# Optimization experiments

Hardware: AMD Instinct MI355X
Metric: run time of the kernel (lower is better)

The kernel has to match this reference:

```python
import jax, jax.numpy as jnp
import numpy as np

N, E, D = 100000, 1600000, 128


def setup_inputs() -> dict:
    key = jax.random.key(0)
    ks = jax.random.split(key, 8)
    s = 1.0 / np.sqrt(D)
    return {
        "x": jax.random.normal(ks[0], (N, D), dtype=jnp.float32),
        "edge_index": jax.random.randint(ks[1], (2, E), 0, N, dtype=jnp.int64),
        "x_prev": jax.random.normal(ks[2], (N, D), dtype=jnp.float32),
        # GCNConv params: weight [in,out], bias [out]
        "W": jax.random.uniform(ks[3], (D, D), jnp.float32, -s, s),
        "b": jnp.zeros((D,), jnp.float32),
        # GRUCell params (torch layout): [3*H, H] gates ordered (r, z, n)
        "W_ih": jax.random.uniform(ks[4], (3 * D, D), jnp.float32, -s, s),
        "W_hh": jax.random.uniform(ks[5], (3 * D, D), jnp.float32, -s, s),
        "b_ih": jax.random.uniform(ks[6], (3 * D,), jnp.float32, -s, s),
        "b_hh": jax.random.uniform(ks[7], (3 * D,), jnp.float32, -s, s),
    }


def _gcn_conv(x, edge_index, W, b):
    n = x.shape[0]
    loop = jnp.arange(n, dtype=edge_index.dtype)
    src = jnp.concatenate([edge_index[0], loop])  # [E+N]
    dst = jnp.concatenate([edge_index[1], loop])
    # symmetric normalization: deg over destinations (incl. self loops)
    deg = jax.ops.segment_sum(jnp.ones_like(dst, dtype=x.dtype), dst, num_segments=n)
    dinv = jnp.where(deg > 0, jax.lax.rsqrt(deg), 0.0)
    norm = dinv[src] * dinv[dst]  # [E+N]
    xw = x @ W  # [N, out]
    msg = xw[src] * norm[:, None]  # gather + scale
    return jax.ops.segment_sum(msg, dst, num_segments=n) + b


def _gru_cell(inp, h, W_ih, W_hh, b_ih, b_hh):
    gi = inp @ W_ih.T + b_ih  # [N, 3H]
    gh = h @ W_hh.T + b_hh
    i_r, i_z, i_n = jnp.split(gi, 3, axis=-1)
    h_r, h_z, h_n = jnp.split(gh, 3, axis=-1)
    r = jax.nn.sigmoid(i_r + h_r)
    z = jax.nn.sigmoid(i_z + h_z)
    ntil = jnp.tanh(i_n + r * h_n)
    return (1.0 - z) * ntil + z * h


def reference(x, edge_index, x_prev, W, b, W_ih, W_hh, b_ih, b_hh):
    h_cur = _gcn_conv(x, edge_index, W, b)
    return _gru_cell(h_cur, x_prev, W_ih, W_hh, b_ih, b_hh)
```

## Files before the change

kernel.cpp:

```cpp
#include <hip/hip_runtime.h>
#include <hip/hip_bf16.h>
#include <math.h>

#define DIM 128
#define PSHIFT 10
#define PSZ 1024
#define CHUNK 2048

typedef __attribute__((ext_vector_type(8))) short bf16x8;
typedef __attribute__((ext_vector_type(4))) float f32x4;
typedef unsigned short u16;
typedef unsigned int u32;
typedef unsigned long long u64;

__device__ __forceinline__ u16 f2bf(float x) {
    u32 u = __builtin_bit_cast(u32, x);
    u += 0x7fff + ((u >> 16) & 1);
    return (u16)(u >> 16);
}
__device__ __forceinline__ float bf2f(u16 h) {
    return __builtin_bit_cast(float, (u32)h << 16);
}


__global__ __launch_bounds__(256) void k_zero(int* __restrict__ p, int n) {
    int i = blockIdx.x * 256 + threadIdx.x;
    if (i < n) p[i] = 0;
}

__global__ __launch_bounds__(256) void k_pcount(const int* __restrict__ edst,
                                                int* __restrict__ pcnt, int E) {
    __shared__ int h[128];
    int t = threadIdx.x;
    if (t < 128) h[t] = 0;
    __syncthreads();
    int stride = gridDim.x * 256;
    for (int e = blockIdx.x * 256 + t; e < E; e += stride)
        atomicAdd(&h[edst[e] >> PSHIFT], 1);
    __syncthreads();
    if (t < 128 && h[t]) atomicAdd(&pcnt[t], h[t]);
}

__global__ __launch_bounds__(256) void k_pscan(const int* __restrict__ pcnt,
                                               int* __restrict__ poff,
                                               int* __restrict__ pfill,
                                               int* __restrict__ rowp,
                                               int P, int N, int E) {
    __shared__ int a[256];
    int t = threadIdx.x;
    int v = (t < P) ? pcnt[t] : 0;
    a[t] = v;
    __syncthreads();
    #pragma unroll
    for (int off = 1; off < 256; off <<= 1) {
        int y = (t >= off) ? a[t - off] : 0;
        __syncthreads();
        a[t] += y;
        __syncthreads();
    }
    int excl = a[t] - v;
    if (t < P) { poff[t] = excl; pfill[t] = excl; }
    if (t == 0) { poff[P] = E; rowp[N] = E; }
}

__global__ __launch_bounds__(256) void k_pscatter(const int* __restrict__ esrc,
                                                  const int* __restrict__ edst,
                                                  int* __restrict__ pfill,
                                                  u64* __restrict__ pbuf, int E) {
    __shared__ int hist[128], sc[128], lofs[128], gbase[128];
    __shared__ u32 ss[CHUNK], sd[CHUNK];
    int t = threadIdx.x;
    int c0 = blockIdx.x * CHUNK;
    int cnt = E - c0; if (cnt > CHUNK) cnt = CHUNK;

    if (t < 128) hist[t] = 0;
    __syncthreads();

    u32 s[8], d[8];
    int p[8], r[8];
    #pragma unroll
    for (int j = 0; j < 8; ++j) {
        int i = j * 256 + t;
        if (i < cnt) {
            s[j] = (u32)esrc[c0 + i];
            d[j] = (u32)edst[c0 + i];
            p[j] = (int)(d[j] >> PSHIFT);
            r[j] = atomicAdd(&hist[p[j]], 1);
        }
    }
    __syncthreads();

    if (t < 128) sc[t] = hist[t];
    __syncthreads();
    #pragma unroll
    for (int off = 1; off < 128; off <<= 1) {
        int y = 0;
        if (t < 128 && t >= off) y = sc[t - off];
        __syncthreads();
        if (t < 128) sc[t] += y;
        __syncthreads();
    }
    if (t < 128) {
        lofs[t] = sc[t] - hist[t];
        if (hist[t] > 0) gbase[t] = atomicAdd(&pfill[t], hist[t]);
    }
    __syncthreads();

    #pragma unroll
    for (int j = 0; j < 8; ++j) {
        int i = j * 256 + t;
        if (i < cnt) {
            int idx = lofs[p[j]] + r[j];
            ss[idx] = s[j];
            sd[idx] = d[j];
        }
    }
    __syncthreads();

    for (int i = t; i < cnt; i += 256) {
        u32 dd = sd[i];
        int pp = (int)(dd >> PSHIFT);
        int gpos = gbase[pp] + (i - lofs[pp]);
        pbuf[gpos] = (u64)ss[i] | ((u64)dd << 32);
    }
}

__global__ __launch_bounds__(256) void k_pfill(const u64* __restrict__ pbuf,
                                               const int* __restrict__ poff,
                                               int* __restrict__ rowp,
                                               int* __restrict__ srcs,
                                               float* __restrict__ dinv, int N) {
    __shared__ int cnt[PSZ];
    __shared__ int wsum[4];
    int p = blockIdx.x, t = threadIdx.x;
    int lane = t & 63, wid = t >> 6;
    int nb0 = p << PSHIFT;
    int ncnt = N - nb0; if (ncnt > PSZ) ncnt = PSZ;
    int b0 = poff[p], b1 = poff[p + 1];
    int bc = b1 - b0;

    for (int i = t; i < PSZ; i += 256) cnt[i] = 0;
    __syncthreads();
    for (int i = t; i < bc; i += 256) {
        u32 d = (u32)(pbuf[b0 + i] >> 32);
        atomicAdd(&cnt[d - nb0], 1);
    }
    __syncthreads();

    int base = t * 4;
    int c[4];
    int ssum = 0;
    #pragma unroll
    for (int j = 0; j < 4; ++j) { c[j] = cnt[base + j]; ssum += c[j]; }
    int incl = ssum;
    #pragma unroll
    for (int off = 1; off < 64; off <<= 1) {
        int y = __shfl_up(incl, off, 64);
        if (lane >= off) incl += y;
    }
    if (lane == 63) wsum[wid] = incl;
    __syncthreads();
    int add = 0;
    for (int w = 0; w < wid; ++w) add += wsum[w];
    int rr = b0 + add + (incl - ssum);
    #pragma unroll
    for (int j = 0; j < 4; ++j) {
        int i = base + j;
        if (i < ncnt) {
            rowp[nb0 + i] = rr;
            dinv[nb0 + i] = rsqrtf((float)(c[j] + 1));
        }
        cnt[i] = rr;
        rr += c[j];
    }
    __syncthreads();

    for (int i = t; i < bc; i += 256) {
        u64 v = pbuf[b0 + i];
        u32 sv = (u32)v;
        u32 d = (u32)(v >> 32);
        int pos = atomicAdd(&cnt[d - nb0], 1);
        srcs[pos] = (int)sv;
    }
}


__global__ __launch_bounds__(256) void k_prepw(const float* __restrict__ W,
                                               const float* __restrict__ Wih,
                                               const float* __restrict__ Whh,
                                               u16* __restrict__ Wt,
                                               u16* __restrict__ Wihb,
                                               u16* __restrict__ Whhb) {
    int i = blockIdx.x * 256 + threadIdx.x;
    if (i < 128 * 128) {
        int k = i >> 7, c = i & 127;
        Wt[c * 128 + k] = f2bf(W[i]);
    }
    if (i < 3 * 128 * 128) {
        Wihb[i] = f2bf(Wih[i]);
        Whhb[i] = f2bf(Whh[i]);
    }
}

__global__ __launch_bounds__(256) void k_cast1(const float4* __restrict__ a,
                                               u32* __restrict__ ab, int n4) {
    int stride = gridDim.x * 256;
    for (int i = blockIdx.x * 256 + threadIdx.x; i < n4; i += stride) {
        float4 v = a[i];
        ab[i * 2 + 0] = (u32)f2bf(v.x) | ((u32)f2bf(v.y) << 16);
        ab[i * 2 + 1] = (u32)f2bf(v.z) | ((u32)f2bf(v.w) << 16);
    }
}


__global__ __launch_bounds__(256) void k_gemm1(const float* __restrict__ X,
                                               const u16* __restrict__ Wt,
                                               u16* __restrict__ XWb, int n) {
    __shared__ u16 Wlds[128 * 128];
    int t = threadIdx.x, w = t >> 6, l = t & 63;
    int lr = l & 15, q = l >> 4;

    for (int cidx = t; cidx < 2048; cidx += 256) {
        int r = cidx >> 4, kc = cidx & 15;
        int dst = r * 128 + ((kc * 8) ^ ((r & 7) << 3));
        *(bf16x8*)(Wlds + dst) = *(const bf16x8*)(Wt + r * 128 + kc * 8);
    }
    __syncthreads();

    int r0 = blockIdx.x * 128;
    int wrow0 = r0 + w * 32;
    int sw = (lr & 7) << 3;
    int ar0 = wrow0 + lr;      if (ar0 > n - 1) ar0 = n - 1;
    int ar1 = wrow0 + 16 + lr; if (ar1 > n - 1) ar1 = n - 1;
    const float* x0 = X + (size_t)ar0 * DIM;
    const float* x1 = X + (size_t)ar1 * DIM;

    f32x4 acc[2][8];
    #pragma unroll
    for (int s = 0; s < 2; ++s)
        #pragma unroll
        for (int c = 0; c < 8; ++c) acc[s][c] = (f32x4){0.f, 0.f, 0.f, 0.f};

    #pragma unroll
    for (int kb = 0; kb < 4; ++kb) {
        int ko = kb * 32 + q * 8;
        float4 f00 = *(const float4*)(x0 + ko), f01 = *(const float4*)(x0 + ko + 4);
        float4 f10 = *(const float4*)(x1 + ko), f11 = *(const float4*)(x1 + ko + 4);
        bf16x8 a0, a1;
        a0[0] = (short)f2bf(f00.x); a0[1] = (short)f2bf(f00.y);
        a0[2] = (short)f2bf(f00.z); a0[3] = (short)f2bf(f00.w);
        a0[4] = (short)f2bf(f01.x); a0[5] = (short)f2bf(f01.y);
        a0[6] = (short)f2bf(f01.z); a0[7] = (short)f2bf(f01.w);
        a1[0] = (short)f2bf(f10.x); a1[1] = (short)f2bf(f10.y);
        a1[2] = (short)f2bf(f10.z); a1[3] = (short)f2bf(f10.w);
        a1[4] = (short)f2bf(f11.x); a1[5] = (short)f2bf(f11.y);
        a1[6] = (short)f2bf(f11.z); a1[7] = (short)f2bf(f11.w);
        int kw = ko ^ sw;
        #pragma unroll
        for (int ct = 0; ct < 8; ++ct) {
            bf16x8 b = *(const bf16x8*)(Wlds + (ct * 16 + lr) * 128 + kw);
            acc[0][ct] = __builtin_amdgcn_mfma_f32_16x16x32_bf16(a0, b, acc[0][ct], 0, 0, 0);
            acc[1][ct] = __builtin_amdgcn_mfma_f32_16x16x32_bf16(a1, b, acc[1][ct], 0, 0, 0);
        }
    }

    #pragma unroll
    for (int s = 0; s < 2; ++s)
        #pragma unroll
        for (int ct = 0; ct < 8; ++ct)
            #pragma unroll
            for (int i = 0; i < 4; ++i) {
                int row = wrow0 + s * 16 + q * 4 + i;
                if (row < n)
                    XWb[(size_t)row * DIM + ct * 16 + lr] = f2bf(acc[s][ct][i]);
            }
}


__global__ __launch_bounds__(256) void k_gather(const u16* __restrict__ XWb,
                                                const float* __restrict__ dinv,
                                                const int* __restrict__ row_ptr,
                                                const int* __restrict__ srcs,
                                                const float* __restrict__ bias,
                                                u16* __restrict__ Hcb, int n) {
    int node = blockIdx.x * 4 + (threadIdx.x >> 6);
    if (node >= n) return;
    int lane = threadIdx.x & 63;
    int c = lane * 2;

    float di = dinv[node];
    u32 sv = *(const u32*)(XWb + (size_t)node * DIM + c);
    float accx = bias[c]     + bf2f((u16)(sv & 0xffff)) * di * di;
    float accy = bias[c + 1] + bf2f((u16)(sv >> 16))    * di * di;

    int e = row_ptr[node], end = row_ptr[node + 1];
    for (; e + 3 < end; e += 4) {
        int s0 = srcs[e], s1 = srcs[e + 1], s2 = srcs[e + 2], s3 = srcs[e + 3];
        float n0 = dinv[s0] * di, n1 = dinv[s1] * di, n2 = dinv[s2] * di, n3 = dinv[s3] * di;
        u32 v0 = *(const u32*)(XWb + (size_t)s0 * DIM + c);
        u32 v1 = *(const u32*)(XWb + (size_t)s1 * DIM + c);
        u32 v2 = *(const u32*)(XWb + (size_t)s2 * DIM + c);
        u32 v3 = *(const u32*)(XWb + (size_t)s3 * DIM + c);
        accx += bf2f((u16)(v0 & 0xffff)) * n0 + bf2f((u16)(v1 & 0xffff)) * n1
              + bf2f((u16)(v2 & 0xffff)) * n2 + bf2f((u16)(v3 & 0xffff)) * n3;
        accy += bf2f((u16)(v0 >> 16)) * n0 + bf2f((u16)(v1 >> 16)) * n1
              + bf2f((u16)(v2 >> 16)) * n2 + bf2f((u16)(v3 >> 16)) * n3;
    }
    for (; e < end; ++e) {
        int s = srcs[e];
        float nrm = dinv[s] * di;
        u32 v = *(const u32*)(XWb + (size_t)s * DIM + c);
        accx += bf2f((u16)(v & 0xffff)) * nrm;
        accy += bf2f((u16)(v >> 16)) * nrm;
    }
    *(u32*)(Hcb + (size_t)node * DIM + c) = (u32)f2bf(accx) | ((u32)f2bf(accy) << 16);
}


__global__ __launch_bounds__(256) void k_gru(const u16* __restrict__ Hcb,
                                             const u16* __restrict__ Xpb,
                                             const u16* __restrict__ Wihb,
                                             const u16* __restrict__ Whhb,
                                             const float* __restrict__ bih,
                                             const float* __restrict__ bhh,
                                             float* __restrict__ Out, int n) {
    __shared__ u16 Wlds[192 * 128];
    int t = threadIdx.x, w = t >> 6, l = t & 63;
    int lr = l & 15, q = l >> 4;
    int cs = blockIdx.x & 3;
    int rb = blockIdx.x >> 2;
    int c0 = cs * 32;
    int r0 = rb * 128;

    for (int cidx = t; cidx < 3072; cidx += 256) {
        int r = cidx >> 4, kc = cidx & 15;
        int m = (r >= 96);
        int rr = m ? r - 96 : r;
        int g = rr >> 5, cc = rr & 31;
        const u16* src = (m ? Whhb : Wihb) + (size_t)((g << 7) + c0 + cc) * DIM + kc * 8;
        int dst = r * 128 + ((kc * 8) ^ ((r & 7) << 3));
        *(bf16x8*)(Wlds + dst) = *(const bf16x8*)src;
    }
    __syncthreads();

    int wrow0 = r0 + w * 32;
    int sw = (lr & 7) << 3;
    int ar0 = wrow0 + lr;      if (ar0 > n - 1) ar0 = n - 1;
    int ar1 = wrow0 + 16 + lr; if (ar1 > n - 1) ar1 = n - 1;
    const u16* hb0 = Hcb + (size_t)ar0 * DIM;
    const u16* hb1 = Hcb + (size_t)ar1 * DIM;
    const u16* xb0 = Xpb + (size_t)ar0 * DIM;
    const u16* xb1 = Xpb + (size_t)ar1 * DIM;

    f32x4 aI[3][2][2], aH[3][2][2];
    #pragma unroll
    for (int g = 0; g < 3; ++g)
        #pragma unroll
        for (int s = 0; s < 2; ++s)
            #pragma unroll
            for (int c = 0; c < 2; ++c) {
                aI[g][s][c] = (f32x4){0.f, 0.f, 0.f, 0.f};
                aH[g][s][c] = (f32x4){0.f, 0.f, 0.f, 0.f};
            }

    #pragma unroll
    for (int kb = 0; kb < 4; ++kb) {
        int ko = kb * 32 + q * 8;
        bf16x8 hA0 = *(const bf16x8*)(hb0 + ko);
        bf16x8 hA1 = *(const bf16x8*)(hb1 + ko);
        bf16x8 xA0 = *(const bf16x8*)(xb0 + ko);
        bf16x8 xA1 = *(const bf16x8*)(xb1 + ko);
        int kw = ko ^ sw;
        #pragma unroll
        for (int g = 0; g < 3; ++g)
            #pragma unroll
            for (int ct = 0; ct < 2; ++ct) {
                int ridx = (g * 32 + ct * 16 + lr) * 128 + kw;
                bf16x8 bI = *(const bf16x8*)(Wlds + ridx);
                bf16x8 bH = *(const bf16x8*)(Wlds + ridx + 96 * 128);
                aI[g][0][ct] = __builtin_amdgcn_mfma_f32_16x16x32_bf16(hA0, bI, aI[g][0][ct], 0, 0, 0);
                aI[g][1][ct] = __builtin_amdgcn_mfma_f32_16x16x32_bf16(hA1, bI, aI[g][1][ct], 0, 0, 0);
                aH[g][0][ct] = __builtin_amdgcn_mfma_f32_16x16x32_bf16(xA0, bH, aH[g][0][ct], 0, 0, 0);
                aH[g][1][ct] = __builtin_amdgcn_mfma_f32_16x16x32_bf16(xA1, bH, aH[g][1][ct], 0, 0, 0);
            }
    }

    #pragma unroll
    for (int ct = 0; ct < 2; ++ct) {
        int j = c0 + ct * 16 + lr;
        float br = bih[j],       bz = bih[128 + j], bn = bih[256 + j];
        float cr = bhh[j],       cz = bhh[128 + j], cn = bhh[256 + j];
        #pragma unroll
        for (int s = 0; s < 2; ++s)
            #pragma unroll
            for (int i = 0; i < 4; ++i) {
                int row = wrow0 + s * 16 + q * 4 + i;
                if (row >= n) continue;
                float ir = aI[0][s][ct][i] + br;
                float iz = aI[1][s][ct][i] + bz;
                float in_ = aI[2][s][ct][i] + bn;
                float hr = aH[0][s][ct][i] + cr;
                float hz = aH[1][s][ct][i] + cz;
                float hn = aH[2][s][ct][i] + cn;
                float rr = 1.f / (1.f + __expf(-(ir + hr)));
                float zz = 1.f / (1.f + __expf(-(iz + hz)));
                float nn = tanhf(in_ + rr * hn);
                float hp = bf2f((u16)Xpb[(size_t)row * DIM + j]);
                Out[(size_t)row * DIM + j] = (1.f - zz) * nn + zz * hp;
            }
    }
}


extern "C" void kernel_launch(void* const* d_in, const int* in_sizes, int n_in,
                              void* d_out, int out_size, void* d_ws, size_t ws_size,
                              hipStream_t stream) {
    const float* x     = (const float*)d_in[0];
    const int*   ei    = (const int*)d_in[1];
    const float* xprev = (const float*)d_in[2];
    const float* W     = (const float*)d_in[3];
    const float* b     = (const float*)d_in[4];
    const float* Wih   = (const float*)d_in[5];
    const float* Whh   = (const float*)d_in[6];
    const float* bih   = (const float*)d_in[7];
    const float* bhh   = (const float*)d_in[8];

    int N = in_sizes[0] / DIM;
    int E = in_sizes[1] / 2;
    int P = (N + PSZ - 1) >> PSHIFT;
    const int* esrc = ei;
    const int* edst = ei + E;

    char* p = (char*)d_ws;
    auto alloc = [&](size_t bytes) {
        char* q = p;
        p += (bytes + 255) & ~(size_t)255;
        return q;
    };
    float* dinv = (float*)alloc((size_t)N * 4);
    int*   rowp = (int*)  alloc((size_t)(N + 1) * 4);
    int*   srcs = (int*)  alloc((size_t)E * 4);
    u16*   Hcb  = (u16*)  alloc((size_t)N * DIM * 2);
    u16*   Xpb  = (u16*)  alloc((size_t)N * DIM * 2);
    u16*   XWb  = (u16*)  alloc((size_t)N * DIM * 2);
    u16*   Wt   = (u16*)  alloc(128 * 128 * 2);
    u16*   Wihb = (u16*)  alloc(3 * 128 * 128 * 2);
    u16*   Whhb = (u16*)  alloc(3 * 128 * 128 * 2);
    int*   pcnt = (int*)  alloc(128 * 4);
    int*   poff = (int*)  alloc(129 * 4);
    int*   pfil = (int*)  alloc(128 * 4);
    u64*   pbuf = (u64*)XWb;
    float* out  = (float*)d_out;

    k_zero    <<<1, 256, 0, stream>>>(pcnt, 128);
    k_pcount  <<<1024, 256, 0, stream>>>(edst, pcnt, E);
    k_pscan   <<<1, 256, 0, stream>>>(pcnt, poff, pfil, rowp, P, N, E);
    int nch = (E + CHUNK - 1) / CHUNK;
    k_pscatter<<<nch, 256, 0, stream>>>(esrc, edst, pfil, pbuf, E);
    k_pfill   <<<P, 256, 0, stream>>>(pbuf, poff, rowp, srcs, dinv, N);
    k_prepw   <<<192, 256, 0, stream>>>(W, Wih, Whh, Wt, Wihb, Whhb);
    int n4 = N * DIM / 4;
    k_cast1   <<<2048, 256, 0, stream>>>((const float4*)xprev, (u32*)Xpb, n4);
    int nrb = (N + 127) / 128;
    k_gemm1   <<<nrb, 256, 0, stream>>>(x, Wt, XWb, N);
    k_gather  <<<(N + 3) / 4, 256, 0, stream>>>(XWb, dinv, rowp, srcs, b, Hcb, N);
    k_gru     <<<nrb * 4, 256, 0, stream>>>(Hcb, Xpb, Wihb, Whhb, bih, bhh, out, N);
}
```

Measured before the change: 310.7 us.

## Split GRU kernel into 8 column slices with XCD-aware block remapping

The GRU kernel now gives each block 16 output columns instead of 32 and launches twice as many blocks. This halves the LDS weight tile (24KB) and the accumulator registers, which should raise occupancy. Block IDs are also remapped so that consecutive logical tiles, which share the same row block, land on the same XCD and can reuse its L2 for the Hc and Xprev rows. The cost is that each row's activations are loaded by 8 blocks instead of 4, and the weight slice is reloaded in every block.

```diff
diff --git a/kernel.cpp b/kernel.cpp
--- a/kernel.cpp
+++ b/kernel.cpp
@@ -324,19 +324,24 @@
                                              const float* __restrict__ bih,
                                              const float* __restrict__ bhh,
                                              float* __restrict__ Out, int n) {
-    __shared__ u16 Wlds[192 * 128];
+    __shared__ u16 Wlds[96 * 128];
     int t = threadIdx.x, w = t >> 6, l = t & 63;
     int lr = l & 15, q = l >> 4;
-    int cs = blockIdx.x & 3;
-    int rb = blockIdx.x >> 2;
-    int c0 = cs * 32;
+
+    int nwg = gridDim.x;
+    int qq = nwg >> 3, rr8 = nwg & 7;
+    int xcd = blockIdx.x & 7, idx = blockIdx.x >> 3;
+    int logical = (xcd < rr8 ? xcd * (qq + 1) : rr8 * (qq + 1) + (xcd - rr8) * qq) + idx;
+    int cs = logical & 7;
+    int rb = logical >> 3;
+    int c0 = cs * 16;
     int r0 = rb * 128;
 
-    for (int cidx = t; cidx < 3072; cidx += 256) {
+    for (int cidx = t; cidx < 1536; cidx += 256) {
         int r = cidx >> 4, kc = cidx & 15;
-        int m = (r >= 96);
-        int rr = m ? r - 96 : r;
-        int g = rr >> 5, cc = rr & 31;
+        int m = (r >= 48);
+        int rr = m ? r - 48 : r;
+        int g = rr >> 4, cc = rr & 15;
         const u16* src = (m ? Whhb : Wihb) + (size_t)((g << 7) + c0 + cc) * DIM + kc * 8;
         int dst = r * 128 + ((kc * 8) ^ ((r & 7) << 3));
         *(bf16x8*)(Wlds + dst) = *(const bf16x8*)src;
@@ -352,16 +357,14 @@
     const u16* xb0 = Xpb + (size_t)ar0 * DIM;
     const u16* xb1 = Xpb + (size_t)ar1 * DIM;
 
-    f32x4 aI[3][2][2], aH[3][2][2];
+    f32x4 aI[3][2], aH[3][2];
     #pragma unroll
     for (int g = 0; g < 3; ++g)
         #pragma unroll
-        for (int s = 0; s < 2; ++s)
-            #pragma unroll
-            for (int c = 0; c < 2; ++c) {
-                aI[g][s][c] = (f32x4){0.f, 0.f, 0.f, 0.f};
-                aH[g][s][c] = (f32x4){0.f, 0.f, 0.f, 0.f};
-            }
+        for (int s = 0; s < 2; ++s) {
+            aI[g][s] = (f32x4){0.f, 0.f, 0.f, 0.f};
+            aH[g][s] = (f32x4){0.f, 0.f, 0.f, 0.f};
+        }
 
     #pragma unroll
     for (int kb = 0; kb < 4; ++kb) {
@@ -372,43 +375,38 @@
         bf16x8 xA1 = *(const bf16x8*)(xb1 + ko);
         int kw = ko ^ sw;
         #pragma unroll
-        for (int g = 0; g < 3; ++g)
-            #pragma unroll
-            for (int ct = 0; ct < 2; ++ct) {
-                int ridx = (g * 32 + ct * 16 + lr) * 128 + kw;
-                bf16x8 bI = *(const bf16x8*)(Wlds + ridx);
-                bf16x8 bH = *(const bf16x8*)(Wlds + ridx + 96 * 128);
-                aI[g][0][ct] = __builtin_amdgcn_mfma_f32_16x16x32_bf16(hA0, bI, aI[g][0][ct], 0, 0, 0);
-                aI[g][1][ct] = __builtin_amdgcn_mfma_f32_16x16x32_bf16(hA1, bI, aI[g][1][ct], 0, 0, 0);
-                aH[g][0][ct] = __builtin_amdgcn_mfma_f32_16x16x32_bf16(xA0, bH, aH[g][0][ct], 0, 0, 0);
-                aH[g][1][ct] = __builtin_amdgcn_mfma_f32_16x16x32_bf16(xA1, bH, aH[g][1][ct], 0, 0, 0);
-            }
-    }
-
-    #pragma unroll
-    for (int ct = 0; ct < 2; ++ct) {
-        int j = c0 + ct * 16 + lr;
-        float br = bih[j],       bz = bih[128 + j], bn = bih[256 + j];
-        float cr = bhh[j],       cz = bhh[128 + j], cn = bhh[256 + j];
-        #pragma unroll
-        for (int s = 0; s < 2; ++s)
-            #pragma unroll
-            for (int i = 0; i < 4; ++i) {
-                int row = wrow0 + s * 16 + q * 4 + i;
-                if (row >= n) continue;
-                float ir = aI[0][s][ct][i] + br;
-                float iz = aI[1][s][ct][i] + bz;
-                float in_ = aI[2][s][ct][i] + bn;
-                float hr = aH[0][s][ct][i] + cr;
-                float hz = aH[1][s][ct][i] + cz;
-                float hn = aH[2][s][ct][i] + cn;
-                float rr = 1.f / (1.f + __expf(-(ir + hr)));
-                float zz = 1.f / (1.f + __expf(-(iz + hz)));
-                float nn = tanhf(in_ + rr * hn);
-                float hp = bf2f((u16)Xpb[(size_t)row * DIM + j]);
-                Out[(size_t)row * DIM + j] = (1.f - zz) * nn + zz * hp;
-            }
-    }
+        for (int g = 0; g < 3; ++g) {
+            int ridx = (g * 16 + lr) * 128 + kw;
+            bf16x8 bI = *(const bf16x8*)(Wlds + ridx);
+            bf16x8 bH = *(const bf16x8*)(Wlds + ridx + 48 * 128);
+            aI[g][0] = __builtin_amdgcn_mfma_f32_16x16x32_bf16(hA0, bI, aI[g][0], 0, 0, 0);
+            aI[g][1] = __builtin_amdgcn_mfma_f32_16x16x32_bf16(hA1, bI, aI[g][1], 0, 0, 0);
+            aH[g][0] = __builtin_amdgcn_mfma_f32_16x16x32_bf16(xA0, bH, aH[g][0], 0, 0, 0);
+            aH[g][1] = __builtin_amdgcn_mfma_f32_16x16x32_bf16(xA1, bH, aH[g][1], 0, 0, 0);
+        }
+    }
+
+    int j = c0 + lr;
+    float br = bih[j],       bz = bih[128 + j], bn = bih[256 + j];
+    float cr = bhh[j],       cz = bhh[128 + j], cn = bhh[256 + j];
+    #pragma unroll
+    for (int s = 0; s < 2; ++s)
+        #pragma unroll
+        for (int i = 0; i < 4; ++i) {
+            int row = wrow0 + s * 16 + q * 4 + i;
+            if (row >= n) continue;
+            float ir = aI[0][s][i] + br;
+            float iz = aI[1][s][i] + bz;
+            float in_ = aI[2][s][i] + bn;
+            float hr = aH[0][s][i] + cr;
+            float hz = aH[1][s][i] + cz;
+            float hn = aH[2][s][i] + cn;
+            float rg = 1.f / (1.f + __expf(-(ir + hr)));
+            float zg = 1.f / (1.f + __expf(-(iz + hz)));
+            float ng = tanhf(in_ + rg * hn);
+            float hp = bf2f((u16)Xpb[(size_t)row * DIM + j]);
+            Out[(size_t)row * DIM + j] = (1.f - zg) * ng + zg * hp;
+        }
 }
 
 
@@ -464,5 +462,5 @@
     int nrb = (N + 127) / 128;
     k_gemm1   <<<nrb, 256, 0, stream>>>(x, Wt, XWb, N);
     k_gather  <<<(N + 3) / 4, 256, 0, stream>>>(XWb, dinv, rowp, srcs, b, Hcb, N);
-    k_gru     <<<nrb * 4, 256, 0, stream>>>(Hcb, Xpb, Wihb, Whhb, bih, bhh, out, N);
-}
+    k_gru     <<<nrb * 8, 256, 0, stream>>>(Hcb, Xpb, Wihb, Whhb, bih, bhh, out, N);
+}
```

Measured after the change: 287.3 us. 1.08x faster.
